# Kernel tuning notes

Hardware: AMD Instinct MI355X
Metric: run time of the kernel (lower is better)

## Reference

```python
import math
import jax, jax.numpy as jnp
import numpy as np

TOP_K = 2
_GELU_C = math.sqrt(2.0 / math.pi)

def gelu_new(x):
    # NewGELU: tanh approximation identical to the torch module
    return 0.5 * x * (1.0 + jnp.tanh(_GELU_C * (x + 0.044715 * x * x * x)))

def setup_inputs() -> dict:
    key = jax.random.key(0)
    ks = jax.random.split(key, 6)
    B, T, C, E, H = 2, 2048, 1024, 8, 4096
    s_in = 1.0 / math.sqrt(C)
    s_hid = 1.0 / math.sqrt(H)
    return {
        "x": jax.random.normal(ks[0], (B, T, C), dtype=jnp.float32),
        "router_w": jax.random.normal(ks[1], (E, C), dtype=jnp.float32) * s_in,
        "w_fc": jax.random.normal(ks[2], (E, C, H), dtype=jnp.float32) * s_in,
        "b_fc": jax.random.normal(ks[3], (E, H), dtype=jnp.float32) * 0.02,
        "w_proj": jax.random.normal(ks[4], (E, H, C), dtype=jnp.float32) * s_hid,
        "b_proj": jax.random.normal(ks[5], (E, C), dtype=jnp.float32) * 0.02,
    }

def reference(x, router_w, w_fc, b_fc, w_proj, b_proj):
    B, T, C = x.shape
    E = router_w.shape[0]
    N = B * T
    xf = x.reshape(N, C)
    # Router: Linear(C, E, bias=False), softmax, top-k, renormalize
    logits = xf @ router_w.T                              # [N, E]
    probs = jax.nn.softmax(logits, axis=-1)
    topk_probs, topk_idx = jax.lax.top_k(probs, TOP_K)    # [N, K]
    topk_probs = topk_probs / jnp.sum(topk_probs, axis=-1, keepdims=True)
    # Dense combine weights: zero for unselected experts -> same math as
    # gather/FFN/index_add over selected tokens (dropout=0).
    combine = jnp.zeros((N, E), dtype=x.dtype).at[
        jnp.arange(N)[:, None], topk_idx].add(topk_probs)  # [N, E]
    # Expert FFN applied per expert (batched GEMMs)
    h = gelu_new(jnp.einsum('nc,ech->neh', xf, w_fc) + b_fc)      # [N, E, H]
    out = jnp.einsum('neh,ehc->nec', h, w_proj) + b_proj          # [N, E, C]
    y = jnp.einsum('nec,ne->nc', out, combine)                    # [N, C]
    return y.reshape(B, T, C)
```

## Files before the change

### kernel.cpp

```cpp
#include <hip/hip_runtime.h>


#define NTOK  4096
#define CDIM  1024
#define HDIM  4096
#define NEXP  8
#define NPC   9216
#define MAXMT 72
#define KB_C  32
#define KB_H  128

typedef _Float16 half8 __attribute__((ext_vector_type(8)));
typedef float    f32x4 __attribute__((ext_vector_type(4)));

#define ASYNC_CP16(gp, lp)                                                         \
  __builtin_amdgcn_global_load_lds(                                                \
      (const __attribute__((address_space(1))) unsigned int*)(gp),                 \
      (__attribute__((address_space(3))) unsigned int*)(lp), 16, 0, 0)

__device__ __forceinline__ float gelu_new(float x) {
    const float c = 0.7978845608028654f;
    return 0.5f * x * (1.0f + tanhf(c * (x + 0.044715f * x * x * x)));
}


__global__ void zero_u32(unsigned int* __restrict__ p, int n) {
    int i = blockIdx.x * 256 + threadIdx.x;
    if (i < n) p[i] = 0u;
}


__global__ __launch_bounds__(256) void router_kernel(
    const float* __restrict__ x, const float* __restrict__ rw,
    int* __restrict__ tok_e, float* __restrict__ tok_w, int* __restrict__ counts)
{
    int wave = threadIdx.x >> 6, lane = threadIdx.x & 63;
    int n = blockIdx.x * 4 + wave;
    const float* xr = x + (size_t)n * CDIM;
    float acc[NEXP];
    #pragma unroll
    for (int e = 0; e < NEXP; ++e) acc[e] = 0.f;
    for (int c = lane; c < CDIM; c += 64) {
        float xv = xr[c];
        #pragma unroll
        for (int e = 0; e < NEXP; ++e) acc[e] = fmaf(xv, rw[e * CDIM + c], acc[e]);
    }
    #pragma unroll
    for (int e = 0; e < NEXP; ++e) {
        float v = acc[e];
        #pragma unroll
        for (int off = 32; off > 0; off >>= 1) v += __shfl_down(v, off);
        acc[e] = v;
    }
    if (lane == 0) {
        float l0 = -3.0e38f, l1 = -3.0e38f; int b0 = 0, b1 = 0;
        #pragma unroll
        for (int e = 0; e < NEXP; ++e) {
            float v = acc[e];
            if (v > l0)      { l1 = l0; b1 = b0; l0 = v; b0 = e; }
            else if (v > l1) { l1 = v; b1 = e; }
        }
        float t  = expf(l1 - l0);
        float w0 = 1.f / (1.f + t);
        float w1 = t  / (1.f + t);
        tok_e[n * 2]     = b0;  tok_e[n * 2 + 1] = b1;
        tok_w[n * 2]     = w0;  tok_w[n * 2 + 1] = w1;
        atomicAdd(&counts[b0], 1);
        atomicAdd(&counts[b1], 1);
    }
}

__global__ void plan_kernel(const int* __restrict__ counts, int* __restrict__ cursors,
                            int* __restrict__ mtiles, int* __restrict__ tile_expert)
{
    if (threadIdx.x == 0 && blockIdx.x == 0) {
        int b = 0;
        for (int e = 0; e < NEXP; ++e) {
            cursors[e] = b;
            int tiles = (counts[e] + 127) >> 7;
            for (int t = 0; t < tiles; ++t) tile_expert[(b >> 7) + t] = e;
            b += tiles << 7;
        }
        *mtiles = b >> 7;
        for (int t = b >> 7; t < MAXMT; ++t) tile_expert[t] = 0;
    }
}

__global__ void assign_kernel(const int* __restrict__ tok_e, const float* __restrict__ tok_w,
                              int* __restrict__ cursors,
                              int* __restrict__ pair_tok, float* __restrict__ pair_gate)
{
    int n = blockIdx.x * 256 + threadIdx.x;
    #pragma unroll
    for (int k = 0; k < 2; ++k) {
        int e = tok_e[n * 2 + k];
        int slot = atomicAdd(&cursors[e], 1);
        pair_tok[slot]  = n;
        pair_gate[slot] = tok_w[n * 2 + k];
    }
}


__global__ __launch_bounds__(256) void gather_x_kernel(
    const float* __restrict__ x, const int* __restrict__ pair_tok,
    _Float16* __restrict__ xg)
{
    int o = blockIdx.x * 256 + threadIdx.x;
    int kb   = o / (NPC * 4);
    int rem  = o - kb * (NPC * 4);
    int slot = rem >> 2;
    int c    = (rem & 3) * 8;
    int tok  = pair_tok[slot];
    const float* src = x + (size_t)tok * CDIM + kb * 32 + c;
    float4 a = *(const float4*)src;
    float4 b = *(const float4*)(src + 4);
    half8 h;
    h[0] = (_Float16)a.x; h[1] = (_Float16)a.y; h[2] = (_Float16)a.z; h[3] = (_Float16)a.w;
    h[4] = (_Float16)b.x; h[5] = (_Float16)b.y; h[6] = (_Float16)b.z; h[7] = (_Float16)b.w;
    *(half8*)(xg + ((size_t)kb * NPC + slot) * 32 + c) = h;
}


__global__ __launch_bounds__(256) void transpose_cvt_kernel(
    const float* __restrict__ w, _Float16* __restrict__ wt, int K, int N)
{
    __shared__ float tile[32][68];
    const int e = blockIdx.z, k0 = blockIdx.y * 32, n0 = blockIdx.x * 64;
    const float* src = w + ((size_t)e * K + k0) * N + n0;
    const int t = threadIdx.x;
    #pragma unroll
    for (int f = t; f < 512; f += 256) {
        int k = f >> 4, nc = (f & 15) * 4;
        *(float4*)&tile[k][nc] = *(const float4*)(src + (size_t)k * N + nc);
    }
    __syncthreads();
    int n = t >> 2, c2 = (t & 3) * 8;
    half8 h;
    #pragma unroll
    for (int q = 0; q < 8; ++q) h[q] = (_Float16)tile[c2 + q][n];
    int KB = K >> 5;
    _Float16* dst = wt + (((size_t)e * KB + (k0 >> 5)) * N + (n0 + n)) * 32 + c2;
    *(half8*)dst = h;
}


__global__ __launch_bounds__(256) void gemm_fc_kernel(
    const _Float16* __restrict__ xg,
    const _Float16* __restrict__ wt,
    const float*    __restrict__ b_fc,
    const int*      __restrict__ tile_expert,
    const int*      __restrict__ mtiles,
    _Float16*       __restrict__ hb)
{
    const int mt = blockIdx.y;
    if (mt >= *mtiles) return;
    const int nt = blockIdx.x;
    const int e  = tile_expert[mt];
    const int m0 = mt << 7, n0 = nt << 7;

    __shared__ _Float16 As[128 * 32];
    __shared__ _Float16 Bs[128 * 32];

    const int tid = threadIdx.x;
    const int lane = tid & 63, wv = tid >> 6;
    const int wm = (wv >> 1) * 64, wn = (wv & 1) * 64;
    const int l16 = lane & 15, lq = lane >> 4;

    const char* gA0 = (const char*)xg + (size_t)m0 * 64;
    const char* gB0 = (const char*)wt + ((size_t)e * KB_C * HDIM + n0) * 64;
    const int soff = wv * 2048 + lane * 16;
    char* lA = (char*)As + wv * 2048;
    char* lB = (char*)Bs + wv * 2048;

    f32x4 acc[4][4];
    #pragma unroll
    for (int i = 0; i < 4; ++i)
        #pragma unroll
        for (int j = 0; j < 4; ++j) { acc[i][j][0]=0.f; acc[i][j][1]=0.f; acc[i][j][2]=0.f; acc[i][j][3]=0.f; }

    for (int kb = 0; kb < KB_C; ++kb) {
        const char* ga = gA0 + (size_t)kb * (NPC * 64) + soff;
        const char* gb = gB0 + (size_t)kb * (HDIM * 64) + soff;
        ASYNC_CP16(ga,        lA);
        ASYNC_CP16(ga + 1024, lA + 1024);
        ASYNC_CP16(gb,        lB);
        ASYNC_CP16(gb + 1024, lB + 1024);
        __syncthreads();
        half8 af[4], bfv[4];
        #pragma unroll
        for (int i = 0; i < 4; ++i) af[i]  = *(const half8*)&As[(wm + i * 16 + l16) * 32 + lq * 8];
        #pragma unroll
        for (int j = 0; j < 4; ++j) bfv[j] = *(const half8*)&Bs[(wn + j * 16 + l16) * 32 + lq * 8];
        #pragma unroll
        for (int i = 0; i < 4; ++i)
            #pragma unroll
            for (int j = 0; j < 4; ++j)
                acc[i][j] = __builtin_amdgcn_mfma_f32_16x16x32_f16(af[i], bfv[j], acc[i][j], 0, 0, 0);
        __syncthreads();
    }

    float bias[4];
    #pragma unroll
    for (int j = 0; j < 4; ++j) bias[j] = b_fc[e * HDIM + n0 + wn + j * 16 + l16];
    #pragma unroll
    for (int i = 0; i < 4; ++i) {
        #pragma unroll
        for (int r = 0; r < 4; ++r) {
            int slot = m0 + wm + i * 16 + lq * 4 + r;
            #pragma unroll
            for (int j = 0; j < 4; ++j) {
                int n = n0 + wn + j * 16 + l16;
                float v = gelu_new(acc[i][j][r] + bias[j]);
                hb[((size_t)(n >> 5) * NPC + slot) * 32 + (n & 31)] = (_Float16)v;
            }
        }
    }
}


__global__ __launch_bounds__(256) void gemm_proj_kernel(
    const _Float16* __restrict__ hb,
    const _Float16* __restrict__ wt,
    const float*    __restrict__ b_proj,
    const int*      __restrict__ pair_tok,
    const float*    __restrict__ pair_gate,
    const int*      __restrict__ tile_expert,
    const int*      __restrict__ mtiles,
    float*          __restrict__ y)
{
    const int mt = blockIdx.y;
    if (mt >= *mtiles) return;
    const int nt = blockIdx.x;
    const int ks = blockIdx.z;
    const int e  = tile_expert[mt];
    const int m0 = mt << 7, n0 = nt << 7;

    __shared__ _Float16 As[128 * 32];
    __shared__ _Float16 Bs[128 * 32];

    const int tid = threadIdx.x;
    const int lane = tid & 63, wv = tid >> 6;
    const int wm = (wv >> 1) * 64, wn = (wv & 1) * 64;
    const int l16 = lane & 15, lq = lane >> 4;

    const char* gA0 = (const char*)hb + (size_t)m0 * 64;
    const char* gB0 = (const char*)wt + ((size_t)e * KB_H * CDIM + n0) * 64;
    const int soff = wv * 2048 + lane * 16;
    char* lA = (char*)As + wv * 2048;
    char* lB = (char*)Bs + wv * 2048;

    f32x4 acc[4][4];
    #pragma unroll
    for (int i = 0; i < 4; ++i)
        #pragma unroll
        for (int j = 0; j < 4; ++j) { acc[i][j][0]=0.f; acc[i][j][1]=0.f; acc[i][j][2]=0.f; acc[i][j][3]=0.f; }

    const int kb_end = ks * 64 + 64;
    for (int kb = ks * 64; kb < kb_end; ++kb) {
        const char* ga = gA0 + (size_t)kb * (NPC * 64) + soff;
        const char* gb = gB0 + (size_t)kb * (CDIM * 64) + soff;
        ASYNC_CP16(ga,        lA);
        ASYNC_CP16(ga + 1024, lA + 1024);
        ASYNC_CP16(gb,        lB);
        ASYNC_CP16(gb + 1024, lB + 1024);
        __syncthreads();
        half8 af[4], bfv[4];
        #pragma unroll
        for (int i = 0; i < 4; ++i) af[i]  = *(const half8*)&As[(wm + i * 16 + l16) * 32 + lq * 8];
        #pragma unroll
        for (int j = 0; j < 4; ++j) bfv[j] = *(const half8*)&Bs[(wn + j * 16 + l16) * 32 + lq * 8];
        #pragma unroll
        for (int i = 0; i < 4; ++i)
            #pragma unroll
            for (int j = 0; j < 4; ++j)
                acc[i][j] = __builtin_amdgcn_mfma_f32_16x16x32_f16(af[i], bfv[j], acc[i][j], 0, 0, 0);
        __syncthreads();
    }

    float bias[4];
    #pragma unroll
    for (int j = 0; j < 4; ++j)
        bias[j] = (ks == 0) ? b_proj[e * CDIM + n0 + wn + j * 16 + l16] : 0.0f;
    #pragma unroll
    for (int i = 0; i < 4; ++i) {
        #pragma unroll
        for (int r = 0; r < 4; ++r) {
            int slot = m0 + wm + i * 16 + lq * 4 + r;
            float g  = pair_gate[slot];
            if (g != 0.0f) {
                int tok = pair_tok[slot];
                float* dst = y + (size_t)tok * CDIM + n0 + wn + l16;
                #pragma unroll
                for (int j = 0; j < 4; ++j)
                    atomicAdd(&dst[j * 16], (acc[i][j][r] + bias[j]) * g);
            }
        }
    }
}


extern "C" void kernel_launch(void* const* d_in, const int* in_sizes, int n_in,
                              void* d_out, int out_size, void* d_ws, size_t ws_size,
                              hipStream_t stream) {
    const float* x   = (const float*)d_in[0];
    const float* rw  = (const float*)d_in[1];
    const float* wfc = (const float*)d_in[2];
    const float* bfc = (const float*)d_in[3];
    const float* wpj = (const float*)d_in[4];
    const float* bpj = (const float*)d_in[5];
    float* y = (float*)d_out;

    char* ws = (char*)d_ws;
    _Float16* xg  = (_Float16*)(ws);
    _Float16* hb  = (_Float16*)(ws + 18874368);
    _Float16* wt  = (_Float16*)(ws + 94371840);
    char* meta = ws + 161480704;
    int*   pair_tok    = (int*)  (meta);
    float* pair_gate   = (float*)(meta + 36864);
    int*   tok_e       = (int*)  (meta + 73728);
    float* tok_w       = (float*)(meta + 106496);
    int*   counts      = (int*)  (meta + 139264);
    int*   cursors     = counts + 8;
    int*   mtiles      = cursors + 8;
    int*   tile_expert = mtiles + 2;

    zero_u32<<<36, 256, 0, stream>>>((unsigned int*)pair_tok, NPC);
    zero_u32<<<36, 256, 0, stream>>>((unsigned int*)pair_gate, NPC);
    zero_u32<<<1, 256, 0, stream>>>((unsigned int*)counts, NEXP);
    zero_u32<<<16384, 256, 0, stream>>>((unsigned int*)y, NTOK * CDIM);

    router_kernel<<<1024, 256, 0, stream>>>(x, rw, tok_e, tok_w, counts);
    plan_kernel<<<1, 64, 0, stream>>>(counts, cursors, mtiles, tile_expert);
    assign_kernel<<<16, 256, 0, stream>>>(tok_e, tok_w, cursors, pair_tok, pair_gate);
    gather_x_kernel<<<KB_C * NPC * 4 / 256, 256, 0, stream>>>(x, pair_tok, xg);

    transpose_cvt_kernel<<<dim3(HDIM / 64, CDIM / 32, NEXP), 256, 0, stream>>>(wfc, wt, CDIM, HDIM);
    gemm_fc_kernel<<<dim3(HDIM / 128, MAXMT), 256, 0, stream>>>(
        xg, wt, bfc, tile_expert, mtiles, hb);

    transpose_cvt_kernel<<<dim3(CDIM / 64, HDIM / 32, NEXP), 256, 0, stream>>>(wpj, wt, HDIM, CDIM);
    gemm_proj_kernel<<<dim3(CDIM / 128, MAXMT, 2), 256, 0, stream>>>(
        hb, wt, bpj, pair_tok, pair_gate, tile_expert, mtiles, y);
}
```

Baseline: 735.7 us.

## Double-buffer LDS tiles in expert GEMMs and merge metadata zeroing kernels

Both expert GEMM kernels now use two LDS buffers per operand. The global-to-LDS async copy for the next K block is issued before computing on the current one, with explicit vmcnt waits and barriers, so load latency overlaps MFMA work. Launch bounds now request 4 blocks per SM. Three small zeroing launches are merged into one. This doubles LDS per block and relies on hand-written waitcnt and barrier asm being correct, and the first compute after a wait also waits on a barrier that may not cover LDS visibility exactly.

```diff
diff --git a/kernel.cpp b/kernel.cpp
--- a/kernel.cpp
+++ b/kernel.cpp
@@ -18,6 +18,10 @@
       (const __attribute__((address_space(1))) unsigned int*)(gp),                 \
       (__attribute__((address_space(3))) unsigned int*)(lp), 16, 0, 0)
 
+#define BAR()     asm volatile("s_barrier" ::: "memory")
+#define WAITVM4() asm volatile("s_waitcnt vmcnt(4)" ::: "memory")
+#define WAITVM0() asm volatile("s_waitcnt vmcnt(0)" ::: "memory")
+
 __device__ __forceinline__ float gelu_new(float x) {
     const float c = 0.7978845608028654f;
     return 0.5f * x * (1.0f + tanhf(c * (x + 0.044715f * x * x * x)));
@@ -27,6 +31,13 @@
 __global__ void zero_u32(unsigned int* __restrict__ p, int n) {
     int i = blockIdx.x * 256 + threadIdx.x;
     if (i < n) p[i] = 0u;
+}
+
+__global__ void zero_meta(unsigned int* __restrict__ pt, unsigned int* __restrict__ pg,
+                          unsigned int* __restrict__ cnt) {
+    int i = blockIdx.x * 256 + threadIdx.x;
+    if (i < NPC) { pt[i] = 0u; pg[i] = 0u; }
+    if (i < NEXP) cnt[i] = 0u;
 }
 
 
@@ -144,7 +155,7 @@
 }
 
 
-__global__ __launch_bounds__(256) void gemm_fc_kernel(
+__global__ __launch_bounds__(256, 4) void gemm_fc_kernel(
     const _Float16* __restrict__ xg,
     const _Float16* __restrict__ wt,
     const float*    __restrict__ b_fc,
@@ -158,8 +169,8 @@
     const int e  = tile_expert[mt];
     const int m0 = mt << 7, n0 = nt << 7;
 
-    __shared__ _Float16 As[128 * 32];
-    __shared__ _Float16 Bs[128 * 32];
+    __shared__ _Float16 As[2][128 * 32];
+    __shared__ _Float16 Bs[2][128 * 32];
 
     const int tid = threadIdx.x;
     const int lane = tid & 63, wv = tid >> 6;
@@ -169,8 +180,8 @@
     const char* gA0 = (const char*)xg + (size_t)m0 * 64;
     const char* gB0 = (const char*)wt + ((size_t)e * KB_C * HDIM + n0) * 64;
     const int soff = wv * 2048 + lane * 16;
-    char* lA = (char*)As + wv * 2048;
-    char* lB = (char*)Bs + wv * 2048;
+    char* lA0 = (char*)As[0] + wv * 2048;  char* lA1 = (char*)As[1] + wv * 2048;
+    char* lB0 = (char*)Bs[0] + wv * 2048;  char* lB1 = (char*)Bs[1] + wv * 2048;
 
     f32x4 acc[4][4];
     #pragma unroll
@@ -178,25 +189,37 @@
         #pragma unroll
         for (int j = 0; j < 4; ++j) { acc[i][j][0]=0.f; acc[i][j][1]=0.f; acc[i][j][2]=0.f; acc[i][j][3]=0.f; }
 
-    for (int kb = 0; kb < KB_C; ++kb) {
+    auto issue = [&](char* lA, char* lB, int kb) {
         const char* ga = gA0 + (size_t)kb * (NPC * 64) + soff;
         const char* gb = gB0 + (size_t)kb * (HDIM * 64) + soff;
         ASYNC_CP16(ga,        lA);
         ASYNC_CP16(ga + 1024, lA + 1024);
         ASYNC_CP16(gb,        lB);
         ASYNC_CP16(gb + 1024, lB + 1024);
-        __syncthreads();
+    };
+    auto compute = [&](const _Float16* Ab, const _Float16* Bb) {
         half8 af[4], bfv[4];
         #pragma unroll
-        for (int i = 0; i < 4; ++i) af[i]  = *(const half8*)&As[(wm + i * 16 + l16) * 32 + lq * 8];
-        #pragma unroll
-        for (int j = 0; j < 4; ++j) bfv[j] = *(const half8*)&Bs[(wn + j * 16 + l16) * 32 + lq * 8];
+        for (int i = 0; i < 4; ++i) af[i]  = *(const half8*)&Ab[(wm + i * 16 + l16) * 32 + lq * 8];
+        #pragma unroll
+        for (int j = 0; j < 4; ++j) bfv[j] = *(const half8*)&Bb[(wn + j * 16 + l16) * 32 + lq * 8];
         #pragma unroll
         for (int i = 0; i < 4; ++i)
             #pragma unroll
             for (int j = 0; j < 4; ++j)
                 acc[i][j] = __builtin_amdgcn_mfma_f32_16x16x32_f16(af[i], bfv[j], acc[i][j], 0, 0, 0);
-        __syncthreads();
+    };
+
+    issue(lA0, lB0, 0);
+    for (int kb = 0; kb < KB_C; kb += 2) {
+        if (kb + 1 < KB_C) { issue(lA1, lB1, kb + 1); WAITVM4(); } else { WAITVM0(); }
+        BAR();
+        compute(As[0], Bs[0]);
+        BAR();
+        if (kb + 2 < KB_C) { issue(lA0, lB0, kb + 2); WAITVM4(); } else { WAITVM0(); }
+        BAR();
+        compute(As[1], Bs[1]);
+        BAR();
     }
 
     float bias[4];
@@ -218,7 +241,7 @@
 }
 
 
-__global__ __launch_bounds__(256) void gemm_proj_kernel(
+__global__ __launch_bounds__(256, 4) void gemm_proj_kernel(
     const _Float16* __restrict__ hb,
     const _Float16* __restrict__ wt,
     const float*    __restrict__ b_proj,
@@ -235,8 +258,8 @@
     const int e  = tile_expert[mt];
     const int m0 = mt << 7, n0 = nt << 7;
 
-    __shared__ _Float16 As[128 * 32];
-    __shared__ _Float16 Bs[128 * 32];
+    __shared__ _Float16 As[2][128 * 32];
+    __shared__ _Float16 Bs[2][128 * 32];
 
     const int tid = threadIdx.x;
     const int lane = tid & 63, wv = tid >> 6;
@@ -246,8 +269,8 @@
     const char* gA0 = (const char*)hb + (size_t)m0 * 64;
     const char* gB0 = (const char*)wt + ((size_t)e * KB_H * CDIM + n0) * 64;
     const int soff = wv * 2048 + lane * 16;
-    char* lA = (char*)As + wv * 2048;
-    char* lB = (char*)Bs + wv * 2048;
+    char* lA0 = (char*)As[0] + wv * 2048;  char* lA1 = (char*)As[1] + wv * 2048;
+    char* lB0 = (char*)Bs[0] + wv * 2048;  char* lB1 = (char*)Bs[1] + wv * 2048;
 
     f32x4 acc[4][4];
     #pragma unroll
@@ -255,26 +278,38 @@
         #pragma unroll
         for (int j = 0; j < 4; ++j) { acc[i][j][0]=0.f; acc[i][j][1]=0.f; acc[i][j][2]=0.f; acc[i][j][3]=0.f; }
 
-    const int kb_end = ks * 64 + 64;
-    for (int kb = ks * 64; kb < kb_end; ++kb) {
+    auto issue = [&](char* lA, char* lB, int kb) {
         const char* ga = gA0 + (size_t)kb * (NPC * 64) + soff;
         const char* gb = gB0 + (size_t)kb * (CDIM * 64) + soff;
         ASYNC_CP16(ga,        lA);
         ASYNC_CP16(ga + 1024, lA + 1024);
         ASYNC_CP16(gb,        lB);
         ASYNC_CP16(gb + 1024, lB + 1024);
-        __syncthreads();
+    };
+    auto compute = [&](const _Float16* Ab, const _Float16* Bb) {
         half8 af[4], bfv[4];
         #pragma unroll
-        for (int i = 0; i < 4; ++i) af[i]  = *(const half8*)&As[(wm + i * 16 + l16) * 32 + lq * 8];
-        #pragma unroll
-        for (int j = 0; j < 4; ++j) bfv[j] = *(const half8*)&Bs[(wn + j * 16 + l16) * 32 + lq * 8];
+        for (int i = 0; i < 4; ++i) af[i]  = *(const half8*)&Ab[(wm + i * 16 + l16) * 32 + lq * 8];
+        #pragma unroll
+        for (int j = 0; j < 4; ++j) bfv[j] = *(const half8*)&Bb[(wn + j * 16 + l16) * 32 + lq * 8];
         #pragma unroll
         for (int i = 0; i < 4; ++i)
             #pragma unroll
             for (int j = 0; j < 4; ++j)
                 acc[i][j] = __builtin_amdgcn_mfma_f32_16x16x32_f16(af[i], bfv[j], acc[i][j], 0, 0, 0);
-        __syncthreads();
+    };
+
+    const int kbeg = ks * 64, kend = kbeg + 64;
+    issue(lA0, lB0, kbeg);
+    for (int kb = kbeg; kb < kend; kb += 2) {
+        if (kb + 1 < kend) { issue(lA1, lB1, kb + 1); WAITVM4(); } else { WAITVM0(); }
+        BAR();
+        compute(As[0], Bs[0]);
+        BAR();
+        if (kb + 2 < kend) { issue(lA0, lB0, kb + 2); WAITVM4(); } else { WAITVM0(); }
+        BAR();
+        compute(As[1], Bs[1]);
+        BAR();
     }
 
     float bias[4];
@@ -324,9 +359,8 @@
     int*   mtiles      = cursors + 8;
     int*   tile_expert = mtiles + 2;
 
-    zero_u32<<<36, 256, 0, stream>>>((unsigned int*)pair_tok, NPC);
-    zero_u32<<<36, 256, 0, stream>>>((unsigned int*)pair_gate, NPC);
-    zero_u32<<<1, 256, 0, stream>>>((unsigned int*)counts, NEXP);
+    zero_meta<<<36, 256, 0, stream>>>((unsigned int*)pair_tok, (unsigned int*)pair_gate,
+                                      (unsigned int*)counts);
     zero_u32<<<16384, 256, 0, stream>>>((unsigned int*)y, NTOK * CDIM);
 
     router_kernel<<<1024, 256, 0, stream>>>(x, rw, tok_e, tok_w, counts);
```

After: 736.3 us. About the same (+0.1%).
